# Optimization experiments

Measured on AMD Instinct MI355X. Metric: run time of the kernel, lower is better.

## Reference

```python
import jax, jax.numpy as jnp
import numpy as np

RES_SCALE = 1.0

def prelu(x, a):
    return jnp.maximum(x, 0) + a * jnp.minimum(x, 0)

def conv1x1_prelu(x, w, b, a):
    # x: [N,C,H,W], w: [O,C], b: [O]
    y = jnp.einsum('nchw,oc->nohw', x, w) + b[None, :, None, None]
    return prelu(y, a)

def setup_inputs() -> dict:
    key = jax.random.key(0)
    ks = jax.random.split(key, 5)
    N, C, H, W = 2, 128, 96, 96
    Cr = C // 2  # reduction = 2
    return {
        'x':  jax.random.normal(ks[0], (N, C, H, W), jnp.float32),
        'w1': jax.random.normal(ks[1], (Cr, C), jnp.float32) * (1.0 / np.sqrt(C)),
        'b1': jnp.zeros((Cr,), jnp.float32),
        'a1': jnp.asarray(0.25, jnp.float32),
        'w2': jax.random.normal(ks[2], (Cr, C), jnp.float32) * (1.0 / np.sqrt(C)),
        'b2': jnp.zeros((Cr,), jnp.float32),
        'a2': jnp.asarray(0.25, jnp.float32),
        'wa': jax.random.normal(ks[3], (C, C), jnp.float32) * (1.0 / np.sqrt(C)),
        'ba': jnp.zeros((C,), jnp.float32),
        'aa': jnp.asarray(0.25, jnp.float32),
    }

def reference(x, w1, b1, a1, w2, b2, a2, wa, ba, aa):
    N, C, H, W = x.shape
    q = conv1x1_prelu(x, w1, b1, a1)   # [N,Cr,H,W]
    k = conv1x1_prelu(x, w2, b2, a2)   # [N,Cr,H,W]
    v = conv1x1_prelu(x, wa, ba, aa)   # [N,C,H,W]
    Cr = q.shape[1]
    L = H * W
    q = q.transpose(0, 2, 3, 1).reshape(N, L, Cr)   # [N,L,Cr]
    k = k.reshape(N, Cr, L)                          # [N,Cr,L]
    score = jax.nn.softmax(jnp.matmul(q, k), axis=2)  # [N,L,L]
    v = v.reshape(N, C, L).transpose(0, 2, 1)        # [N,L,C]
    out = jnp.matmul(score, v)                        # [N,L,C]
    out = out.transpose(0, 2, 1).reshape(N, C, H, W)
    return out + RES_SCALE * x
```

## Files before the change

### kernel.cpp

```cpp
#include <hip/hip_runtime.h>

#define N_  2
#define C_  128
#define CR_ 64
#define H_  96
#define W_  96
#define L_  (H_*W_)
#define QBLK 128
#define KVBLK 64
#define NQB (L_/QBLK)
#define SPLITS 8
#define TILES_PER ((L_/KVBLK)/SPLITS)
#define NCHUNK (N_*NQB*SPLITS)
#define LOG2E 1.44269504088896f

typedef short bf16x8 __attribute__((ext_vector_type(8)));
typedef float f32x4  __attribute__((ext_vector_type(4)));

static __device__ __forceinline__ float exp2_fast(float x) {
    return __builtin_amdgcn_exp2f(x);
}

static __device__ __forceinline__ unsigned short f2bf(float f) {
    unsigned u = __builtin_bit_cast(unsigned, f);
    unsigned rounding = 0x7FFFu + ((u >> 16) & 1u);
    return (unsigned short)((u + rounding) >> 16);
}

static __device__ __forceinline__ unsigned cvt_pk_bf16(float lo, float hi) {
    unsigned r;
    asm("v_cvt_pk_bf16_f32 %0, %1, %2" : "=v"(r) : "v"(lo), "v"(hi));
    return r;
}

static __device__ __forceinline__ float bf2f(unsigned short s) {
    return __builtin_bit_cast(float, ((unsigned)s) << 16);
}

static __device__ __forceinline__ int sigma_(int r) {
    return (r & 0x23) | ((r & 0x0C) << 1) | ((r & 0x10) >> 2);
}

#define GLD16(G, Ld) __builtin_amdgcn_global_load_lds( \
    (const __attribute__((address_space(1))) void*)(G), \
    (__attribute__((address_space(3))) void*)(Ld), 16, 0, 0)

__global__ __launch_bounds__(256) void wconv_kernel(
    const float* __restrict__ w1, const float* __restrict__ b1, const float* __restrict__ a1,
    const float* __restrict__ w2, const float* __restrict__ b2, const float* __restrict__ a2,
    const float* __restrict__ wa, const float* __restrict__ ba, const float* __restrict__ aa,
    unsigned short* __restrict__ Wbf,
    float* __restrict__ bias, float* __restrict__ alpha, float* __restrict__ scale)
{
    const int idx = blockIdx.x * 256 + threadIdx.x;
    const int o = idx >> 7, k = idx & 127;
    float wv;
    if (o < 64)       wv = w1[o*C_ + k];
    else if (o < 128) wv = w2[(o-64)*C_ + k];
    else              wv = wa[(o-128)*C_ + k];
    Wbf[idx] = f2bf(wv);
    if (blockIdx.x == 0) {
        int t = threadIdx.x;
        float b, a, sc;
        if (t < 64)       { b = b1[t];       a = a1[0]; sc = LOG2E; }
        else if (t < 128) { b = b2[t-64];    a = a2[0]; sc = 1.0f; }
        else              { b = ba[t-128];   a = aa[0]; sc = 1.0f; }
        bias[t] = b; alpha[t] = a; scale[t] = sc;
    }
}

__global__ __launch_bounds__(256) void proj_mfma_kernel(
    const float* __restrict__ x,
    const unsigned short* __restrict__ Wbf,
    const float* __restrict__ bias,
    const float* __restrict__ alpha,
    const float* __restrict__ scale,
    unsigned short* __restrict__ qkv)
{
    __shared__ alignas(16) unsigned char xs[64 * 256];

    const int blk  = blockIdx.x;
    const int n    = blk / (L_/64);
    const int i0   = (blk % (L_/64)) * 64;
    const float* xb = x + (size_t)n * C_ * L_;
    const int tid  = threadIdx.x;
    const int wv_  = tid >> 6;
    const int lane = tid & 63;
    const int lhi  = lane >> 4;
    const int llo  = lane & 15;

    {
        const int i = lane;
        #pragma unroll
        for (int p = 0; p < 8; p++) {
            int c0 = wv_*4 + p*16;
            float v0 = xb[(size_t)(c0+0)*L_ + i0 + i];
            float v1 = xb[(size_t)(c0+1)*L_ + i0 + i];
            float v2 = xb[(size_t)(c0+2)*L_ + i0 + i];
            float v3 = xb[(size_t)(c0+3)*L_ + i0 + i];
            uint2 pk2;
            pk2.x = cvt_pk_bf16(v0, v1);
            pk2.y = cvt_pk_bf16(v2, v3);
            int byte = i*256 + ((((c0 >> 3) ^ (i & 7))) << 4) + (c0 & 7) * 2;
            *reinterpret_cast<uint2*>(xs + byte) = pk2;
        }
    }
    __syncthreads();

    bf16x8 xf[4][4];
    #pragma unroll
    for (int it = 0; it < 4; it++) {
        int i = it*16 + llo;
        #pragma unroll
        for (int ks = 0; ks < 4; ks++) {
            int byte = i*256 + (((ks*4 + lhi) ^ (i & 7)) << 4);
            xf[it][ks] = *reinterpret_cast<const bf16x8*>(xs + byte);
        }
    }

    unsigned short* q_t = qkv;
    unsigned short* k_t = qkv + (size_t)N_ * L_ * CR_;
    unsigned short* v   = qkv + (size_t)2 * N_ * L_ * CR_;
    unsigned short* qtb = q_t + (size_t)n * L_ * CR_;
    unsigned short* ktb = k_t + (size_t)n * L_ * CR_;
    unsigned short* vb  = v   + (size_t)n * C_ * L_;

    #pragma unroll
    for (int oo = 0; oo < 2; oo++) {
        const int ot = wv_*2 + oo;
        const unsigned short* wrow = Wbf + (size_t)(ot*16 + llo) * 128;
        bf16x8 wf[4];
        #pragma unroll
        for (int ks = 0; ks < 4; ks++)
            wf[ks] = *reinterpret_cast<const bf16x8*>(wrow + ks*32 + lhi*8);
        f32x4 acc[4];
        #pragma unroll
        for (int it = 0; it < 4; it++) acc[it] = f32x4{0.f, 0.f, 0.f, 0.f};
        #pragma unroll
        for (int ks = 0; ks < 4; ks++)
            #pragma unroll
            for (int it = 0; it < 4; it++)
                acc[it] = __builtin_amdgcn_mfma_f32_16x16x32_bf16(wf[ks], xf[it][ks], acc[it], 0, 0, 0);

        const int ob = ot*16 + lhi*4;
        const float4 b4 = *reinterpret_cast<const float4*>(bias  + ob);
        const float4 a4 = *reinterpret_cast<const float4*>(alpha + ob);
        const float4 s4 = *reinterpret_cast<const float4*>(scale + ob);
        unsigned short* dst = (ot < 4) ? qtb : ktb;
        const int col = (ot & 3)*16 + lhi*4;
        #pragma unroll
        for (int it = 0; it < 4; it++) {
            int i = i0 + it*16 + llo;
            float y0 = acc[it][0] + b4.x; y0 = (fmaxf(y0,0.f) + a4.x*fminf(y0,0.f))*s4.x;
            float y1 = acc[it][1] + b4.y; y1 = (fmaxf(y1,0.f) + a4.y*fminf(y1,0.f))*s4.y;
            float y2 = acc[it][2] + b4.z; y2 = (fmaxf(y2,0.f) + a4.z*fminf(y2,0.f))*s4.z;
            float y3 = acc[it][3] + b4.w; y3 = (fmaxf(y3,0.f) + a4.w*fminf(y3,0.f))*s4.w;
            uint2 pk2;
            pk2.x = cvt_pk_bf16(y0, y1);
            pk2.y = cvt_pk_bf16(y2, y3);
            *reinterpret_cast<uint2*>(dst + (size_t)i * CR_ + col) = pk2;
        }
    }

    #pragma unroll
    for (int oo = 0; oo < 2; oo++) {
        const int ot2 = wv_*2 + oo;
        const int op  = ot2*16 + llo;
        const unsigned short* wrow = Wbf + (size_t)(128 + op) * 128;
        bf16x8 wf[4];
        #pragma unroll
        for (int ks = 0; ks < 4; ks++)
            wf[ks] = *reinterpret_cast<const bf16x8*>(wrow + ks*32 + lhi*8);
        f32x4 acc[4];
        #pragma unroll
        for (int it = 0; it < 4; it++) acc[it] = f32x4{0.f, 0.f, 0.f, 0.f};
        #pragma unroll
        for (int ks = 0; ks < 4; ks++)
            #pragma unroll
            for (int it = 0; it < 4; it++)
                acc[it] = __builtin_amdgcn_mfma_f32_16x16x32_bf16(xf[it][ks], wf[ks], acc[it], 0, 0, 0);

        const float b = bias[128 + op];
        const float a = alpha[128 + op];
        #pragma unroll
        for (int it = 0; it < 4; it++) {
            float y0 = acc[it][0] + b; y0 = fmaxf(y0,0.f) + a*fminf(y0,0.f);
            float y1 = acc[it][1] + b; y1 = fmaxf(y1,0.f) + a*fminf(y1,0.f);
            float y2 = acc[it][2] + b; y2 = fmaxf(y2,0.f) + a*fminf(y2,0.f);
            float y3 = acc[it][3] + b; y3 = fmaxf(y3,0.f) + a*fminf(y3,0.f);
            uint2 pk2;
            pk2.x = cvt_pk_bf16(y0, y1);
            pk2.y = cvt_pk_bf16(y2, y3);
            *reinterpret_cast<uint2*>(vb + (size_t)op * L_ + i0 + it*16 + lhi*4) = pk2;
        }
    }
}

__global__ __launch_bounds__(256, 3) void attn_kernel(
    const unsigned short* __restrict__ qkv,
    unsigned short* __restrict__ o_part,
    float* __restrict__ l_part)
{
    __shared__ alignas(16) unsigned char kv_lds[2][24*1024];

    const unsigned short* q_t = qkv;
    const unsigned short* k_t = qkv + (size_t)N_ * L_ * CR_;
    const unsigned short* v   = qkv + (size_t)2 * N_ * L_ * CR_;

    const int blk  = blockIdx.x;
    const int n    = blk / (NQB * SPLITS);
    const int rem  = blk % (NQB * SPLITS);
    const int qbi  = rem / SPLITS;
    const int s    = rem % SPLITS;
    const int qb   = qbi * QBLK;
    const int tid  = threadIdx.x;
    const int wave = tid >> 6;
    const int lane = tid & 63;
    const int lhi  = lane >> 4;
    const int llo  = lane & 15;

    const int jb_beg = s * TILES_PER * KVBLK;
    const int jb_end = jb_beg + TILES_PER * KVBLK;

    const unsigned short* qtb = q_t + (size_t)n * L_ * CR_;
    const unsigned short* ktb = k_t + (size_t)n * L_ * CR_;
    const unsigned short* vb  = v   + (size_t)n * C_ * L_;

    bf16x8 qf[2][2];
    #pragma unroll
    for (int st = 0; st < 2; st++) {
        int row = qb + wave * 32 + st * 16 + llo;
        #pragma unroll
        for (int ks = 0; ks < 2; ks++)
            qf[st][ks] = *reinterpret_cast<const bf16x8*>(qtb + (size_t)row * CR_ + ks*32 + lhi*8);
    }

    bf16x8 ones_f;
    #pragma unroll
    for (int e = 0; e < 8; e++) ones_f[e] = (short)0x3F80;

    const int l8 = lane >> 3;
    const int l7 = (lane & 7) * 16;
    const int rho0 = wave*16 + l8;
    const int rho1 = rho0 + 8;
    const unsigned short* kbase0 = ktb + (size_t)sigma_(rho0) * CR_ + ((l7 ^ ((rho0 & 7) << 4)) >> 1);
    const unsigned short* kbase1 = ktb + (size_t)sigma_(rho1) * CR_ + ((l7 ^ ((rho1 & 7) << 4)) >> 1);
    const unsigned short* vbase[4];
    #pragma unroll
    for (int vt = 0; vt < 4; vt++) {
        int c = wave*32 + vt*8 + l8;
        vbase[vt] = vb + (size_t)c * L_ + ((l7 ^ (l8 << 4)) >> 1);
    }

    #define STAGE(b, jb_) do {                                                   \
        GLD16(kbase0 + (size_t)(jb_) * CR_, &kv_lds[b][(wave*2+0)*1024 + 0]);    \
        GLD16(kbase1 + (size_t)(jb_) * CR_, &kv_lds[b][(wave*2+1)*1024 + 0]);    \
        GLD16(vbase[0] + (jb_), &kv_lds[b][8192 + (wave*4+0)*1024]);             \
        GLD16(vbase[1] + (jb_), &kv_lds[b][8192 + (wave*4+1)*1024]);             \
        GLD16(vbase[2] + (jb_), &kv_lds[b][8192 + (wave*4+2)*1024]);             \
        GLD16(vbase[3] + (jb_), &kv_lds[b][8192 + (wave*4+3)*1024]);             \
    } while (0)

    f32x4 o_acc[2][8];
    #pragma unroll
    for (int st = 0; st < 2; st++)
        #pragma unroll
        for (int ct = 0; ct < 8; ct++) o_acc[st][ct] = f32x4{0.f, 0.f, 0.f, 0.f};
    f32x4 acc_l[2];
    acc_l[0] = f32x4{0.f, 0.f, 0.f, 0.f};
    acc_l[1] = f32x4{0.f, 0.f, 0.f, 0.f};

    int cur = 0;
    STAGE(0, jb_beg);
    __syncthreads();

    for (int jb = jb_beg; jb < jb_end; jb += KVBLK) {
        if (jb + KVBLK < jb_end) STAGE(cur ^ 1, jb + KVBLK);

        const unsigned char* kbuf = &kv_lds[cur][0];
        const unsigned char* vbuf = &kv_lds[cur][8192];

        f32x4 sacc[2][4];
        #pragma unroll
        for (int st = 0; st < 2; st++)
            #pragma unroll
            for (int jt = 0; jt < 4; jt++) sacc[st][jt] = f32x4{0.f, 0.f, 0.f, 0.f};
        __builtin_amdgcn_s_setprio(1);
        #pragma unroll
        for (int ks = 0; ks < 2; ks++) {
            #pragma unroll
            for (int jt = 0; jt < 4; jt++) {
                int rho  = jt*16 + llo;
                int colb = ks*64 + lhi*16;
                bf16x8 kf = *reinterpret_cast<const bf16x8*>(
                    kbuf + rho*128 + (colb ^ ((rho & 7) << 4)));
                sacc[0][jt] = __builtin_amdgcn_mfma_f32_16x16x32_bf16(kf, qf[0][ks], sacc[0][jt], 0, 0, 0);
                sacc[1][jt] = __builtin_amdgcn_mfma_f32_16x16x32_bf16(kf, qf[1][ks], sacc[1][jt], 0, 0, 0);
            }
        }
        __builtin_amdgcn_s_setprio(0);

        #pragma unroll
        for (int st = 0; st < 2; st++)
            #pragma unroll
            for (int jt = 0; jt < 4; jt++)
                #pragma unroll
                for (int r = 0; r < 4; r++)
                    sacc[st][jt][r] = exp2_fast(sacc[st][jt][r]);

        __builtin_amdgcn_s_setprio(1);
        #pragma unroll
        for (int ks = 0; ks < 2; ks++) {
            unsigned pw0[4], pw1[4];
            pw0[0] = cvt_pk_bf16(sacc[0][2*ks][0],   sacc[0][2*ks][1]);
            pw0[1] = cvt_pk_bf16(sacc[0][2*ks][2],   sacc[0][2*ks][3]);
            pw0[2] = cvt_pk_bf16(sacc[0][2*ks+1][0], sacc[0][2*ks+1][1]);
            pw0[3] = cvt_pk_bf16(sacc[0][2*ks+1][2], sacc[0][2*ks+1][3]);
            pw1[0] = cvt_pk_bf16(sacc[1][2*ks][0],   sacc[1][2*ks][1]);
            pw1[1] = cvt_pk_bf16(sacc[1][2*ks][2],   sacc[1][2*ks][3]);
            pw1[2] = cvt_pk_bf16(sacc[1][2*ks+1][0], sacc[1][2*ks+1][1]);
            pw1[3] = cvt_pk_bf16(sacc[1][2*ks+1][2], sacc[1][2*ks+1][3]);
            bf16x8 pf0 = *reinterpret_cast<const bf16x8*>(&pw0[0]);
            bf16x8 pf1 = *reinterpret_cast<const bf16x8*>(&pw1[0]);
            acc_l[0] = __builtin_amdgcn_mfma_f32_16x16x32_bf16(ones_f, pf0, acc_l[0], 0, 0, 0);
            acc_l[1] = __builtin_amdgcn_mfma_f32_16x16x32_bf16(ones_f, pf1, acc_l[1], 0, 0, 0);
            #pragma unroll
            for (int ct = 0; ct < 8; ct++) {
                int c = ct*16 + llo;
                int colb = ks*64 + lhi*16;
                bf16x8 vf = *reinterpret_cast<const bf16x8*>(
                    vbuf + c*128 + (colb ^ ((c & 7) << 4)));
                o_acc[0][ct] = __builtin_amdgcn_mfma_f32_16x16x32_bf16(vf, pf0, o_acc[0][ct], 0, 0, 0);
                o_acc[1][ct] = __builtin_amdgcn_mfma_f32_16x16x32_bf16(vf, pf1, o_acc[1][ct], 0, 0, 0);
            }
        }
        __builtin_amdgcn_s_setprio(0);

        __syncthreads();
        cur ^= 1;
    }
    #undef STAGE

    unsigned short* ob = o_part + (size_t)blk * (QBLK*C_);
    float* lb = l_part + (size_t)blk * QBLK;
    #pragma unroll
    for (int st = 0; st < 2; st++) {
        int i_loc = wave*32 + st*16 + llo;
        #pragma unroll
        for (int ct = 0; ct < 8; ct++) {
            int c0 = ct*16 + lhi*4;
            uint2 pkd;
            pkd.x = cvt_pk_bf16(o_acc[st][ct][0], o_acc[st][ct][1]);
            pkd.y = cvt_pk_bf16(o_acc[st][ct][2], o_acc[st][ct][3]);
            *reinterpret_cast<uint2*>(ob + (size_t)i_loc * C_ + c0) = pkd;
        }
        if (lhi == 0) lb[i_loc] = acc_l[st][0];
    }
}

__global__ __launch_bounds__(256) void combine_kernel(
    const unsigned short* __restrict__ o_part,
    const float* __restrict__ l_part,
    const float* __restrict__ x,
    float* __restrict__ out)
{
    __shared__ float invl[32];

    const int blk  = blockIdx.x;
    const int part = blk & 3;
    const int qbi  = (blk >> 2) % NQB;
    const int n    = blk / (4 * NQB);
    const int tid  = threadIdx.x;
    const int i0   = part * 32;

    const size_t pbase = (size_t)(n*NQB + qbi) * SPLITS;

    if (tid < 32) {
        float lt = 0.f;
        for (int s = 0; s < SPLITS; s++)
            lt += l_part[(pbase + s) * QBLK + i0 + tid];
        invl[tid] = 1.0f / lt;
    }
    __syncthreads();

    const int il = tid & 31;
    const int cg = tid >> 5;

    float acc[16];
    #pragma unroll
    for (int k = 0; k < 16; k++) acc[k] = 0.f;

    for (int s = 0; s < SPLITS; s++) {
        const unsigned short* src = o_part + (pbase + s) * (QBLK*C_)
                                  + (size_t)(i0 + il) * C_ + cg*16;
        bf16x8 v0 = *reinterpret_cast<const bf16x8*>(src);
        bf16x8 v1 = *reinterpret_cast<const bf16x8*>(src + 8);
        #pragma unroll
        for (int k = 0; k < 8; k++) acc[k]     += bf2f((unsigned short)v0[k]);
        #pragma unroll
        for (int k = 0; k < 8; k++) acc[8 + k] += bf2f((unsigned short)v1[k]);
    }

    const float nv = invl[il];
    const int ig = qbi*QBLK + i0 + il;
    const float* xb = x   + (size_t)n * C_ * L_;
    float*       ob = out + (size_t)n * C_ * L_;
    #pragma unroll
    for (int k = 0; k < 16; k++) {
        int c = cg*16 + k;
        ob[(size_t)c * L_ + ig] = acc[k] * nv + xb[(size_t)c * L_ + ig];
    }
}

extern "C" void kernel_launch(void* const* d_in, const int* in_sizes, int n_in,
                              void* d_out, int out_size, void* d_ws, size_t ws_size,
                              hipStream_t stream) {
    const float* x  = (const float*)d_in[0];
    const float* w1 = (const float*)d_in[1];
    const float* b1 = (const float*)d_in[2];
    const float* a1 = (const float*)d_in[3];
    const float* w2 = (const float*)d_in[4];
    const float* b2 = (const float*)d_in[5];
    const float* a2 = (const float*)d_in[6];
    const float* wa = (const float*)d_in[7];
    const float* ba = (const float*)d_in[8];
    const float* aa = (const float*)d_in[9];
    float* out = (float*)d_out;

    unsigned short* qkv = (unsigned short*)d_ws;
    size_t qkv_bytes = ((size_t)2*N_*L_*CR_ + (size_t)N_*C_*L_) * 2;
    size_t off = (qkv_bytes + 255) & ~(size_t)255;

    unsigned short* o_part = (unsigned short*)((char*)d_ws + off);
    size_t o_elems = (size_t)NCHUNK * QBLK * C_;
    float* l_part = (float*)(o_part + o_elems);
    float* tail   = l_part + (size_t)NCHUNK * QBLK;
    unsigned short* Wbf = (unsigned short*)tail;
    float* bias  = (float*)(Wbf + 256*128);
    float* alpha = bias + 256;
    float* scale = alpha + 256;

    wconv_kernel<<<128, 256, 0, stream>>>(w1, b1, a1, w2, b2, a2, wa, ba, aa,
                                          Wbf, bias, alpha, scale);
    proj_mfma_kernel<<<N_ * (L_/64), 256, 0, stream>>>(x, Wbf, bias, alpha, scale, qkv);
    attn_kernel<<<NCHUNK, 256, 0, stream>>>(qkv, o_part, l_part);
    combine_kernel<<<N_ * NQB * 4, 256, 0, stream>>>(o_part, l_part, x, out);
}
```

Baseline: 98.96 us.

## Fuse weight conversion into projection kernel and halve projection tile size

Drops the separate weight-conversion kernel launch. The projection kernel now reads the fp32 weights, biases and alphas directly and converts them to bf16 in registers. The projection tile shrinks from 64 to 32 positions, doubling the block count so more blocks run in parallel. The cost is that every block re-reads and re-converts the fp32 weights, giving more redundant global and L2 traffic per output.

```diff
diff --git a/kernel.cpp b/kernel.cpp
--- a/kernel.cpp
+++ b/kernel.cpp
@@ -21,12 +21,6 @@
     return __builtin_amdgcn_exp2f(x);
 }
 
-static __device__ __forceinline__ unsigned short f2bf(float f) {
-    unsigned u = __builtin_bit_cast(unsigned, f);
-    unsigned rounding = 0x7FFFu + ((u >> 16) & 1u);
-    return (unsigned short)((u + rounding) >> 16);
-}
-
 static __device__ __forceinline__ unsigned cvt_pk_bf16(float lo, float hi) {
     unsigned r;
     asm("v_cvt_pk_bf16_f32 %0, %1, %2" : "=v"(r) : "v"(lo), "v"(hi));
@@ -45,43 +39,29 @@
     (const __attribute__((address_space(1))) void*)(G), \
     (__attribute__((address_space(3))) void*)(Ld), 16, 0, 0)
 
-__global__ __launch_bounds__(256) void wconv_kernel(
+static __device__ __forceinline__ bf16x8 w8_from_f32(const float* p) {
+    float4 a = *reinterpret_cast<const float4*>(p);
+    float4 b = *reinterpret_cast<const float4*>(p + 4);
+    union { unsigned u[4]; bf16x8 v; } r;
+    r.u[0] = cvt_pk_bf16(a.x, a.y);
+    r.u[1] = cvt_pk_bf16(a.z, a.w);
+    r.u[2] = cvt_pk_bf16(b.x, b.y);
+    r.u[3] = cvt_pk_bf16(b.z, b.w);
+    return r.v;
+}
+
+__global__ __launch_bounds__(256) void proj_mfma_kernel(
+    const float* __restrict__ x,
     const float* __restrict__ w1, const float* __restrict__ b1, const float* __restrict__ a1,
     const float* __restrict__ w2, const float* __restrict__ b2, const float* __restrict__ a2,
     const float* __restrict__ wa, const float* __restrict__ ba, const float* __restrict__ aa,
-    unsigned short* __restrict__ Wbf,
-    float* __restrict__ bias, float* __restrict__ alpha, float* __restrict__ scale)
-{
-    const int idx = blockIdx.x * 256 + threadIdx.x;
-    const int o = idx >> 7, k = idx & 127;
-    float wv;
-    if (o < 64)       wv = w1[o*C_ + k];
-    else if (o < 128) wv = w2[(o-64)*C_ + k];
-    else              wv = wa[(o-128)*C_ + k];
-    Wbf[idx] = f2bf(wv);
-    if (blockIdx.x == 0) {
-        int t = threadIdx.x;
-        float b, a, sc;
-        if (t < 64)       { b = b1[t];       a = a1[0]; sc = LOG2E; }
-        else if (t < 128) { b = b2[t-64];    a = a2[0]; sc = 1.0f; }
-        else              { b = ba[t-128];   a = aa[0]; sc = 1.0f; }
-        bias[t] = b; alpha[t] = a; scale[t] = sc;
-    }
-}
-
-__global__ __launch_bounds__(256) void proj_mfma_kernel(
-    const float* __restrict__ x,
-    const unsigned short* __restrict__ Wbf,
-    const float* __restrict__ bias,
-    const float* __restrict__ alpha,
-    const float* __restrict__ scale,
     unsigned short* __restrict__ qkv)
 {
-    __shared__ alignas(16) unsigned char xs[64 * 256];
+    __shared__ alignas(16) unsigned char xs[32 * 256];
 
     const int blk  = blockIdx.x;
-    const int n    = blk / (L_/64);
-    const int i0   = (blk % (L_/64)) * 64;
+    const int n    = blk / (L_/32);
+    const int i0   = (blk % (L_/32)) * 32;
     const float* xb = x + (size_t)n * C_ * L_;
     const int tid  = threadIdx.x;
     const int wv_  = tid >> 6;
@@ -89,11 +69,14 @@
     const int lhi  = lane >> 4;
     const int llo  = lane & 15;
 
+    const float alpha_q = a1[0], alpha_k = a2[0], alpha_v = aa[0];
+
     {
-        const int i = lane;
-        #pragma unroll
-        for (int p = 0; p < 8; p++) {
-            int c0 = wv_*4 + p*16;
+        const int i = lane & 31;
+        const int g = lane >> 5;
+        #pragma unroll
+        for (int p = 0; p < 4; p++) {
+            int c0 = (p*8 + wv_*2 + g) * 4;
             float v0 = xb[(size_t)(c0+0)*L_ + i0 + i];
             float v1 = xb[(size_t)(c0+1)*L_ + i0 + i];
             float v2 = xb[(size_t)(c0+2)*L_ + i0 + i];
@@ -107,9 +90,9 @@
     }
     __syncthreads();
 
-    bf16x8 xf[4][4];
-    #pragma unroll
-    for (int it = 0; it < 4; it++) {
+    bf16x8 xf[2][4];
+    #pragma unroll
+    for (int it = 0; it < 2; it++) {
         int i = it*16 + llo;
         #pragma unroll
         for (int ks = 0; ks < 4; ks++) {
@@ -127,34 +110,38 @@
 
     #pragma unroll
     for (int oo = 0; oo < 2; oo++) {
-        const int ot = wv_*2 + oo;
-        const unsigned short* wrow = Wbf + (size_t)(ot*16 + llo) * 128;
+        const int ot  = wv_*2 + oo;
+        const int row = ot*16 + llo;
+        const float* wsrc = (row < 64) ? (w1 + (size_t)row * C_)
+                                       : (w2 + (size_t)(row - 64) * C_);
         bf16x8 wf[4];
         #pragma unroll
         for (int ks = 0; ks < 4; ks++)
-            wf[ks] = *reinterpret_cast<const bf16x8*>(wrow + ks*32 + lhi*8);
-        f32x4 acc[4];
-        #pragma unroll
-        for (int it = 0; it < 4; it++) acc[it] = f32x4{0.f, 0.f, 0.f, 0.f};
-        #pragma unroll
-        for (int ks = 0; ks < 4; ks++)
-            #pragma unroll
-            for (int it = 0; it < 4; it++)
-                acc[it] = __builtin_amdgcn_mfma_f32_16x16x32_bf16(wf[ks], xf[it][ks], acc[it], 0, 0, 0);
+            wf[ks] = w8_from_f32(wsrc + ks*32 + lhi*8);
+
+        f32x4 acc[2];
+        acc[0] = f32x4{0.f, 0.f, 0.f, 0.f};
+        acc[1] = f32x4{0.f, 0.f, 0.f, 0.f};
+        #pragma unroll
+        for (int ks = 0; ks < 4; ks++) {
+            acc[0] = __builtin_amdgcn_mfma_f32_16x16x32_bf16(wf[ks], xf[0][ks], acc[0], 0, 0, 0);
+            acc[1] = __builtin_amdgcn_mfma_f32_16x16x32_bf16(wf[ks], xf[1][ks], acc[1], 0, 0, 0);
+        }
 
         const int ob = ot*16 + lhi*4;
-        const float4 b4 = *reinterpret_cast<const float4*>(bias  + ob);
-        const float4 a4 = *reinterpret_cast<const float4*>(alpha + ob);
-        const float4 s4 = *reinterpret_cast<const float4*>(scale + ob);
+        float4 b4;
+        float av, sc;
+        if (ot < 4) { b4 = *reinterpret_cast<const float4*>(b1 + ob);      av = alpha_q; sc = LOG2E; }
+        else        { b4 = *reinterpret_cast<const float4*>(b2 + ob - 64); av = alpha_k; sc = 1.0f; }
         unsigned short* dst = (ot < 4) ? qtb : ktb;
         const int col = (ot & 3)*16 + lhi*4;
         #pragma unroll
-        for (int it = 0; it < 4; it++) {
+        for (int it = 0; it < 2; it++) {
             int i = i0 + it*16 + llo;
-            float y0 = acc[it][0] + b4.x; y0 = (fmaxf(y0,0.f) + a4.x*fminf(y0,0.f))*s4.x;
-            float y1 = acc[it][1] + b4.y; y1 = (fmaxf(y1,0.f) + a4.y*fminf(y1,0.f))*s4.y;
-            float y2 = acc[it][2] + b4.z; y2 = (fmaxf(y2,0.f) + a4.z*fminf(y2,0.f))*s4.z;
-            float y3 = acc[it][3] + b4.w; y3 = (fmaxf(y3,0.f) + a4.w*fminf(y3,0.f))*s4.w;
+            float y0 = acc[it][0] + b4.x; y0 = (fmaxf(y0,0.f) + av*fminf(y0,0.f))*sc;
+            float y1 = acc[it][1] + b4.y; y1 = (fmaxf(y1,0.f) + av*fminf(y1,0.f))*sc;
+            float y2 = acc[it][2] + b4.z; y2 = (fmaxf(y2,0.f) + av*fminf(y2,0.f))*sc;
+            float y3 = acc[it][3] + b4.w; y3 = (fmaxf(y3,0.f) + av*fminf(y3,0.f))*sc;
             uint2 pk2;
             pk2.x = cvt_pk_bf16(y0, y1);
             pk2.y = cvt_pk_bf16(y2, y3);
@@ -166,28 +153,28 @@
     for (int oo = 0; oo < 2; oo++) {
         const int ot2 = wv_*2 + oo;
         const int op  = ot2*16 + llo;
-        const unsigned short* wrow = Wbf + (size_t)(128 + op) * 128;
+        const float* wsrc = wa + (size_t)op * C_;
         bf16x8 wf[4];
         #pragma unroll
         for (int ks = 0; ks < 4; ks++)
-            wf[ks] = *reinterpret_cast<const bf16x8*>(wrow + ks*32 + lhi*8);
-        f32x4 acc[4];
-        #pragma unroll
-        for (int it = 0; it < 4; it++) acc[it] = f32x4{0.f, 0.f, 0.f, 0.f};
-        #pragma unroll
-        for (int ks = 0; ks < 4; ks++)
-            #pragma unroll
-            for (int it = 0; it < 4; it++)
-                acc[it] = __builtin_amdgcn_mfma_f32_16x16x32_bf16(xf[it][ks], wf[ks], acc[it], 0, 0, 0);
-
-        const float b = bias[128 + op];
-        const float a = alpha[128 + op];
-        #pragma unroll
-        for (int it = 0; it < 4; it++) {
-            float y0 = acc[it][0] + b; y0 = fmaxf(y0,0.f) + a*fminf(y0,0.f);
-            float y1 = acc[it][1] + b; y1 = fmaxf(y1,0.f) + a*fminf(y1,0.f);
-            float y2 = acc[it][2] + b; y2 = fmaxf(y2,0.f) + a*fminf(y2,0.f);
-            float y3 = acc[it][3] + b; y3 = fmaxf(y3,0.f) + a*fminf(y3,0.f);
+            wf[ks] = w8_from_f32(wsrc + ks*32 + lhi*8);
+
+        f32x4 acc[2];
+        acc[0] = f32x4{0.f, 0.f, 0.f, 0.f};
+        acc[1] = f32x4{0.f, 0.f, 0.f, 0.f};
+        #pragma unroll
+        for (int ks = 0; ks < 4; ks++) {
+            acc[0] = __builtin_amdgcn_mfma_f32_16x16x32_bf16(xf[0][ks], wf[ks], acc[0], 0, 0, 0);
+            acc[1] = __builtin_amdgcn_mfma_f32_16x16x32_bf16(xf[1][ks], wf[ks], acc[1], 0, 0, 0);
+        }
+
+        const float b = ba[op];
+        #pragma unroll
+        for (int it = 0; it < 2; it++) {
+            float y0 = acc[it][0] + b; y0 = fmaxf(y0,0.f) + alpha_v*fminf(y0,0.f);
+            float y1 = acc[it][1] + b; y1 = fmaxf(y1,0.f) + alpha_v*fminf(y1,0.f);
+            float y2 = acc[it][2] + b; y2 = fmaxf(y2,0.f) + alpha_v*fminf(y2,0.f);
+            float y3 = acc[it][3] + b; y3 = fmaxf(y3,0.f) + alpha_v*fminf(y3,0.f);
             uint2 pk2;
             pk2.x = cvt_pk_bf16(y0, y1);
             pk2.y = cvt_pk_bf16(y2, y3);
@@ -434,15 +421,8 @@
     unsigned short* o_part = (unsigned short*)((char*)d_ws + off);
     size_t o_elems = (size_t)NCHUNK * QBLK * C_;
     float* l_part = (float*)(o_part + o_elems);
-    float* tail   = l_part + (size_t)NCHUNK * QBLK;
-    unsigned short* Wbf = (unsigned short*)tail;
-    float* bias  = (float*)(Wbf + 256*128);
-    float* alpha = bias + 256;
-    float* scale = alpha + 256;
-
-    wconv_kernel<<<128, 256, 0, stream>>>(w1, b1, a1, w2, b2, a2, wa, ba, aa,
-                                          Wbf, bias, alpha, scale);
-    proj_mfma_kernel<<<N_ * (L_/64), 256, 0, stream>>>(x, Wbf, bias, alpha, scale, qkv);
+
+    proj_mfma_kernel<<<N_ * (L_/32), 256, 0, stream>>>(x, w1, b1, a1, w2, b2, a2, wa, ba, aa, qkv);
     attn_kernel<<<NCHUNK, 256, 0, stream>>>(qkv, o_part, l_part);
     combine_kernel<<<N_ * NQB * 4, 256, 0, stream>>>(o_part, l_part, x, out);
 }
```

Result: no change. 99.34 us (+0.4%).
